# Performance work log

Hardware: AMD Instinct MI355X
Metric: run time of the kernel (lower is better)

The kernel has to match this reference:

```python
import jax, jax.numpy as jnp
import numpy as np

IN_F, OUT_F = 1024, 1024
GRID_SIZE, SPLINE_ORDER = 5, 3
BATCH = 4096
GRID_LO, GRID_HI = -1.0, 1.0


def _make_grid():
    h = (GRID_HI - GRID_LO) / GRID_SIZE
    g = jnp.arange(-SPLINE_ORDER, GRID_SIZE + SPLINE_ORDER + 1, dtype=jnp.float32) * h + GRID_LO  # [12]
    return jnp.broadcast_to(g, (IN_F, g.shape[0]))  # [in, 12]


def setup_inputs() -> dict:
    key = jax.random.key(0)
    k1, k2, k3 = jax.random.split(key, 3)
    x = jax.random.normal(k1, (BATCH, IN_F), dtype=jnp.float32)
    base_weight = jax.random.normal(k2, (OUT_F, IN_F), dtype=jnp.float32) * (1.0 / np.sqrt(IN_F))
    spline_weight = jax.random.normal(k3, (OUT_F, IN_F, GRID_SIZE + SPLINE_ORDER), dtype=jnp.float32) * 0.1
    spline_scaler = jnp.ones((OUT_F, IN_F), dtype=jnp.float32)
    grid = _make_grid()
    return {"x": x, "base_weight": base_weight, "spline_weight": spline_weight,
            "spline_scaler": spline_scaler, "grid": grid}


def b_splines(x, grid):
    # x: [B, in], grid: [in, 12] -> bases: [B, in, grid_size+spline_order]
    xe = x[..., None]  # [B, in, 1]
    bases = ((xe >= grid[:, :-1]) & (xe < grid[:, 1:])).astype(x.dtype)  # [B, in, 11]
    for k in range(1, SPLINE_ORDER + 1):
        t0 = grid[:, :-(k + 1)]
        t1 = grid[:, k:-1]
        t2 = grid[:, k + 1:]
        t3 = grid[:, 1:-k]
        bases = ((xe - t0) / (t1 - t0 + 1e-8) * bases[..., :-1]
                 + (t2 - xe) / (t2 - t3 + 1e-8) * bases[..., 1:])
    return bases


def reference(x, base_weight, spline_weight, spline_scaler, grid):
    base_output = jax.nn.silu(x) @ base_weight.T  # [B, out]
    spline_basis = b_splines(x, grid)             # [B, in, 8]
    spline_output = jnp.einsum('bij,oij,oi->bo', spline_basis, spline_weight, spline_scaler)
    return base_output + spline_output
```

## Files before the change

### kernel.cpp

```cpp
#include <hip/hip_runtime.h>
#include <hip/hip_bf16.h>
#include <stdint.h>
#include <stddef.h>

#define IN_F     1024
#define OUT_F    1024
#define BATCH    4096
#define NSPLINE  8
#define KDIM     (IN_F * 9)
#define GRIDPTS  12

typedef __bf16 bf16;
typedef __bf16 bf16x8 __attribute__((ext_vector_type(8)));
typedef float  f32x4  __attribute__((ext_vector_type(4)));

__global__ __launch_bounds__(256) void build_A(const float* __restrict__ x,
                                               const float* __restrict__ grid,
                                               bf16* __restrict__ A)
{
    __shared__ float g[GRIDPTS];
    __shared__ float rec[33];
    if (threadIdx.x < GRIDPTS) g[threadIdx.x] = grid[threadIdx.x];
    __syncthreads();
    if (threadIdx.x < 33) {
        const int k = threadIdx.x / 11 + 1;
        const int j = threadIdx.x % 11;
        if (j + k <= 11) rec[threadIdx.x] = 1.0f / (g[j + k] - g[j] + 1e-8f);
    }
    __syncthreads();

    const int idx = blockIdx.x * 256 + threadIdx.x;
    const int b = idx >> 10;
    const int i = idx & 1023;
    const float xv = x[idx];

    float bs[11];
#pragma unroll
    for (int j = 0; j < 11; ++j)
        bs[j] = (xv >= g[j] && xv < g[j + 1]) ? 1.0f : 0.0f;

#pragma unroll
    for (int k = 1; k <= 3; ++k) {
        const float* rk = &rec[(k - 1) * 11];
#pragma unroll
        for (int j = 0; j < 10; ++j) {
            if (j <= 10 - k) {
                bs[j] = (xv - g[j]) * rk[j] * bs[j]
                      + (g[j + k + 1] - xv) * rk[j + 1] * bs[j + 1];
            }
        }
    }

    const float si = xv / (1.0f + __expf(-xv));

    bf16* rowp = A + (size_t)b * KDIM;
    rowp[i] = (bf16)si;
#pragma unroll
    for (int j = 0; j < NSPLINE; ++j)
        rowp[(size_t)(j + 1) * IN_F + i] = (bf16)bs[j];
}

__global__ __launch_bounds__(256) void pack_W(const float* __restrict__ bw,
                                              const float* __restrict__ sw,
                                              const float* __restrict__ sc,
                                              bf16* __restrict__ W)
{
    const int idx = blockIdx.x * 256 + threadIdx.x;
    const int i = idx & 1023;
    const float s = sc[idx];

    bf16* rowp = W + (size_t)(idx >> 10) * KDIM;
    rowp[i] = (bf16)bw[idx];

    const float4* swv = (const float4*)(sw + (size_t)idx * NSPLINE);
    const float4 w0 = swv[0];
    const float4 w1 = swv[1];
    rowp[(size_t)1 * IN_F + i] = (bf16)(w0.x * s);
    rowp[(size_t)2 * IN_F + i] = (bf16)(w0.y * s);
    rowp[(size_t)3 * IN_F + i] = (bf16)(w0.z * s);
    rowp[(size_t)4 * IN_F + i] = (bf16)(w0.w * s);
    rowp[(size_t)5 * IN_F + i] = (bf16)(w1.x * s);
    rowp[(size_t)6 * IN_F + i] = (bf16)(w1.y * s);
    rowp[(size_t)7 * IN_F + i] = (bf16)(w1.z * s);
    rowp[(size_t)8 * IN_F + i] = (bf16)(w1.w * s);
}

#define BM8 256
#define BN8 256
#define BK8 64

#define GLOAD_LDS16(gp, lp)                                                          \
    __builtin_amdgcn_global_load_lds((const __attribute__((address_space(1))) void*)(gp), \
                                     (__attribute__((address_space(3))) void*)(lp), 16, 0, 0)

__global__ __launch_bounds__(512, 2) void gemm8(const bf16* __restrict__ A,
                                                const bf16* __restrict__ B,
                                                float* __restrict__ C,
                                                int kLen)
{
    __shared__ bf16 lds[8 * 8192];

    const int tid  = threadIdx.x;
    const int wave = tid >> 6;
    const int lane = tid & 63;

    const int nwg  = gridDim.x;
    const int q    = nwg >> 3;
    const int wgid = (blockIdx.x & 7) * q + (blockIdx.x >> 3);
    const int nxy  = (BATCH / BM8) * (OUT_F / BN8);
    const int z    = wgid / nxy;
    const int rem  = wgid - z * nxy;
    const int by   = rem >> 4;
    const int bx   = rem & 15;

    const int bm = bx * BM8;
    const int bn = by * BN8;
    const int kBase = z * kLen;
    C += (size_t)z * BATCH * OUT_F;

    const int wr = (wave >> 2) * 128;
    const int wc = (wave & 3) * 64;

    f32x4 acc[8][4] = {};

    const int NT   = kLen / BK8;
    const int hmax = 4 * NT;

    const int srow = tid >> 2;
    const int sch  = (((tid & 3) ^ ((tid >> 3) & 3))) * 8;
    const bf16* baseA = A + (size_t)(bm + srow) * KDIM + kBase + sch;
    const bf16* baseB = B + (size_t)(bn + srow) * KDIM + kBase + sch;
    const size_t rstep = (size_t)128 * KDIM;
    bf16* ldsw = &lds[wave * 512];

    auto stage = [&](int h) {
        if (h < hmax) {
            const int t   = h >> 2;
            const int th  = h & 3;
            const int kof = t * BK8 + ((th >> 1) ? 32 : 0);
            const bf16* src = (th & 1) ? baseB : baseA;
            bf16* l0 = ldsw + (h & 7) * 8192;
            GLOAD_LDS16(src + kof, l0);
            GLOAD_LDS16(src + kof + rstep, l0 + 4096);
        }
    };

    for (int h = 0; h < 6; ++h) stage(h);
    asm volatile("s_waitcnt vmcnt(4)" ::: "memory");
    __builtin_amdgcn_s_barrier();

    const int rowk = lane & 15;
    const int kc   = lane >> 4;

#define LDSFRAG(slot, row) (*(const bf16x8*)&lds[(slot) * 8192 + (row) * 32 + \
                               ((kc ^ (((row) >> 1) & 3)) * 8)])

    for (int t = 0; t < NT; ++t) {
        const int h0  = 4 * t;
        const int sA0 = (h0 + 0) & 7, sB0 = (h0 + 1) & 7;
        const int sA1 = (h0 + 2) & 7, sB1 = (h0 + 3) & 7;
        bf16x8 a[4], b[4];

#pragma unroll
        for (int m = 0; m < 4; ++m) a[m] = LDSFRAG(sA0, wr + m * 16 + rowk);
#pragma unroll
        for (int n = 0; n < 4; ++n) b[n] = LDSFRAG(sB0, wc + n * 16 + rowk);
        stage(h0 + 6);
        __builtin_amdgcn_s_barrier();
        asm volatile("s_waitcnt lgkmcnt(0)" ::: "memory");
        __builtin_amdgcn_sched_barrier(0);
        __builtin_amdgcn_s_setprio(1);
#pragma unroll
        for (int m = 0; m < 4; ++m)
#pragma unroll
            for (int n = 0; n < 4; ++n)
                acc[m][n] = __builtin_amdgcn_mfma_f32_16x16x32_bf16(a[m], b[n], acc[m][n], 0, 0, 0);
        __builtin_amdgcn_s_setprio(0);
        __builtin_amdgcn_s_barrier();

#pragma unroll
        for (int m = 0; m < 4; ++m) a[m] = LDSFRAG(sA0, wr + 64 + m * 16 + rowk);
        stage(h0 + 7);
        __builtin_amdgcn_s_barrier();
        asm volatile("s_waitcnt lgkmcnt(0)" ::: "memory");
        __builtin_amdgcn_sched_barrier(0);
        __builtin_amdgcn_s_setprio(1);
#pragma unroll
        for (int m = 0; m < 4; ++m)
#pragma unroll
            for (int n = 0; n < 4; ++n)
                acc[4 + m][n] = __builtin_amdgcn_mfma_f32_16x16x32_bf16(a[m], b[n], acc[4 + m][n], 0, 0, 0);
        __builtin_amdgcn_s_setprio(0);
        __builtin_amdgcn_s_barrier();

#pragma unroll
        for (int m = 0; m < 4; ++m) a[m] = LDSFRAG(sA1, wr + m * 16 + rowk);
#pragma unroll
        for (int n = 0; n < 4; ++n) b[n] = LDSFRAG(sB1, wc + n * 16 + rowk);
        stage(h0 + 8);
        __builtin_amdgcn_s_barrier();
        asm volatile("s_waitcnt lgkmcnt(0)" ::: "memory");
        __builtin_amdgcn_sched_barrier(0);
        __builtin_amdgcn_s_setprio(1);
#pragma unroll
        for (int m = 0; m < 4; ++m)
#pragma unroll
            for (int n = 0; n < 4; ++n)
                acc[m][n] = __builtin_amdgcn_mfma_f32_16x16x32_bf16(a[m], b[n], acc[m][n], 0, 0, 0);
        __builtin_amdgcn_s_setprio(0);
        __builtin_amdgcn_s_barrier();

#pragma unroll
        for (int m = 0; m < 4; ++m) a[m] = LDSFRAG(sA1, wr + 64 + m * 16 + rowk);
        stage(h0 + 9);
        __builtin_amdgcn_s_barrier();
        asm volatile("s_waitcnt lgkmcnt(0)" ::: "memory");
        __builtin_amdgcn_sched_barrier(0);
        __builtin_amdgcn_s_setprio(1);
#pragma unroll
        for (int m = 0; m < 4; ++m)
#pragma unroll
            for (int n = 0; n < 4; ++n)
                acc[4 + m][n] = __builtin_amdgcn_mfma_f32_16x16x32_bf16(a[m], b[n], acc[4 + m][n], 0, 0, 0);
        __builtin_amdgcn_s_setprio(0);
        if (t < NT - 2)       asm volatile("s_waitcnt vmcnt(4)" ::: "memory");
        else if (t == NT - 2) asm volatile("s_waitcnt vmcnt(0)" ::: "memory");
        __builtin_amdgcn_s_barrier();
    }
#undef LDSFRAG

    const int ccol = lane & 15;
    const int crow = (lane >> 4) * 4;
#pragma unroll
    for (int mf = 0; mf < 8; ++mf) {
#pragma unroll
        for (int nf = 0; nf < 4; ++nf) {
            float* cp = C + (size_t)(bm + wr + mf * 16 + crow) * OUT_F + (bn + wc + nf * 16 + ccol);
#pragma unroll
            for (int r = 0; r < 4; ++r)
                cp[(size_t)r * OUT_F] = acc[mf][nf][r];
        }
    }
}

__global__ __launch_bounds__(256) void reduce_partials(const float4* __restrict__ P,
                                                       float4* __restrict__ out,
                                                       int nPart, int n4)
{
    const int stride = gridDim.x * 256;
    for (int i = blockIdx.x * 256 + threadIdx.x; i < n4; i += stride) {
        float4 s = P[i];
        for (int p = 1; p < nPart; ++p) {
            const float4 q = P[(size_t)p * n4 + i];
            s.x += q.x; s.y += q.y; s.z += q.z; s.w += q.w;
        }
        out[i] = s;
    }
}

extern "C" void kernel_launch(void* const* d_in, const int* in_sizes, int n_in,
                              void* d_out, int out_size, void* d_ws, size_t ws_size,
                              hipStream_t stream)
{
    const float* x  = (const float*)d_in[0];
    const float* bw = (const float*)d_in[1];
    const float* sw = (const float*)d_in[2];
    const float* sc = (const float*)d_in[3];
    const float* gr = (const float*)d_in[4];
    float* out = (float*)d_out;

    bf16* A = (bf16*)d_ws;
    bf16* W = A + (size_t)BATCH * KDIM;
    float* parts = (float*)(W + (size_t)OUT_F * KDIM);

    const size_t baseBytes = ((size_t)BATCH + OUT_F) * KDIM * sizeof(bf16);
    const size_t cBytes    = (size_t)BATCH * OUT_F * sizeof(float);

    int split = 1;
    if (ws_size >= baseBytes + 4 * cBytes)      split = 4;
    else if (ws_size >= baseBytes + 2 * cBytes) split = 2;

    build_A<<<(BATCH * IN_F) / 256, 256, 0, stream>>>(x, gr, A);
    pack_W<<<(OUT_F * IN_F) / 256, 256, 0, stream>>>(bw, sw, sc, W);

    const int nblk = (BATCH / BM8) * (OUT_F / BN8) * split;
    float* gemmOut = (split > 1) ? parts : out;
    gemm8<<<nblk, 512, 0, stream>>>(A, W, gemmOut, KDIM / split);

    if (split > 1) {
        const int n4 = BATCH * OUT_F / 4;
        reduce_partials<<<2048, 256, 0, stream>>>((const float4*)parts, (float4*)out,
                                                  split, n4);
    }
}
```

Baseline: 122.9 us.

## Double-buffer LDS fragments in registers to overlap reads with MFMA

Restructures the GEMM main loop so LDS fragment reads for the next MFMA block are issued before the current MFMA block runs. Extra register buffers (a2, b2) and a prologue load make this possible, and the barrier plus lgkmcnt(0) wait before each compute phase is removed. It also hoists the swizzled k-offset into a precomputed value. The aim is to hide LDS latency and cut barrier stalls, at the cost of higher VGPR pressure and reliance on compiler-inserted waits for the LDS reads to complete.

```diff
diff --git a/kernel.cpp b/kernel.cpp
--- a/kernel.cpp
+++ b/kernel.cpp
@@ -114,7 +114,7 @@
     const int bx   = rem & 15;
 
     const int bm = bx * BM8;
-    const int bn = by * BN8;
+    const int bcol = by * BN8;
     const int kBase = z * kLen;
     C += (size_t)z * BATCH * OUT_F;
 
@@ -129,7 +129,7 @@
     const int srow = tid >> 2;
     const int sch  = (((tid & 3) ^ ((tid >> 3) & 3))) * 8;
     const bf16* baseA = A + (size_t)(bm + srow) * KDIM + kBase + sch;
-    const bf16* baseB = B + (size_t)(bn + srow) * KDIM + kBase + sch;
+    const bf16* baseB = B + (size_t)(bcol + srow) * KDIM + kBase + sch;
     const size_t rstep = (size_t)128 * KDIM;
     bf16* ldsw = &lds[wave * 512];
 
@@ -151,23 +151,24 @@
 
     const int rowk = lane & 15;
     const int kc   = lane >> 4;
-
-#define LDSFRAG(slot, row) (*(const bf16x8*)&lds[(slot) * 8192 + (row) * 32 + \
-                               ((kc ^ (((row) >> 1) & 3)) * 8)])
+    const int kxor = (kc ^ ((rowk >> 1) & 3)) * 8;
+
+#define LDSFRAG(slot, row) (*(const bf16x8*)&lds[(slot) * 8192 + (row) * 32 + kxor])
+
+    bf16x8 a[4], b[4], a2[4], b2[4];
+#pragma unroll
+    for (int m = 0; m < 4; ++m) a[m] = LDSFRAG(0, wr + m * 16 + rowk);
+#pragma unroll
+    for (int n = 0; n < 4; ++n) b[n] = LDSFRAG(1, wc + n * 16 + rowk);
 
     for (int t = 0; t < NT; ++t) {
         const int h0  = 4 * t;
-        const int sA0 = (h0 + 0) & 7, sB0 = (h0 + 1) & 7;
+        const int sA0 = (h0 + 0) & 7;
         const int sA1 = (h0 + 2) & 7, sB1 = (h0 + 3) & 7;
-        bf16x8 a[4], b[4];
-
-#pragma unroll
-        for (int m = 0; m < 4; ++m) a[m] = LDSFRAG(sA0, wr + m * 16 + rowk);
-#pragma unroll
-        for (int n = 0; n < 4; ++n) b[n] = LDSFRAG(sB0, wc + n * 16 + rowk);
+
         stage(h0 + 6);
-        __builtin_amdgcn_s_barrier();
-        asm volatile("s_waitcnt lgkmcnt(0)" ::: "memory");
+#pragma unroll
+        for (int m = 0; m < 4; ++m) a2[m] = LDSFRAG(sA0, wr + 64 + m * 16 + rowk);
         __builtin_amdgcn_sched_barrier(0);
         __builtin_amdgcn_s_setprio(1);
 #pragma unroll
@@ -178,53 +179,52 @@
         __builtin_amdgcn_s_setprio(0);
         __builtin_amdgcn_s_barrier();
 
-#pragma unroll
-        for (int m = 0; m < 4; ++m) a[m] = LDSFRAG(sA0, wr + 64 + m * 16 + rowk);
         stage(h0 + 7);
-        __builtin_amdgcn_s_barrier();
-        asm volatile("s_waitcnt lgkmcnt(0)" ::: "memory");
-        __builtin_amdgcn_sched_barrier(0);
-        __builtin_amdgcn_s_setprio(1);
-#pragma unroll
-        for (int m = 0; m < 4; ++m)
-#pragma unroll
-            for (int n = 0; n < 4; ++n)
-                acc[4 + m][n] = __builtin_amdgcn_mfma_f32_16x16x32_bf16(a[m], b[n], acc[4 + m][n], 0, 0, 0);
-        __builtin_amdgcn_s_setprio(0);
-        __builtin_amdgcn_s_barrier();
-
 #pragma unroll
         for (int m = 0; m < 4; ++m) a[m] = LDSFRAG(sA1, wr + m * 16 + rowk);
 #pragma unroll
-        for (int n = 0; n < 4; ++n) b[n] = LDSFRAG(sB1, wc + n * 16 + rowk);
+        for (int n = 0; n < 4; ++n) b2[n] = LDSFRAG(sB1, wc + n * 16 + rowk);
+        __builtin_amdgcn_sched_barrier(0);
+        __builtin_amdgcn_s_setprio(1);
+#pragma unroll
+        for (int m = 0; m < 4; ++m)
+#pragma unroll
+            for (int n = 0; n < 4; ++n)
+                acc[4 + m][n] = __builtin_amdgcn_mfma_f32_16x16x32_bf16(a2[m], b[n], acc[4 + m][n], 0, 0, 0);
+        __builtin_amdgcn_s_setprio(0);
+        __builtin_amdgcn_s_barrier();
+
         stage(h0 + 8);
-        __builtin_amdgcn_s_barrier();
-        asm volatile("s_waitcnt lgkmcnt(0)" ::: "memory");
-        __builtin_amdgcn_sched_barrier(0);
-        __builtin_amdgcn_s_setprio(1);
-#pragma unroll
-        for (int m = 0; m < 4; ++m)
-#pragma unroll
-            for (int n = 0; n < 4; ++n)
-                acc[m][n] = __builtin_amdgcn_mfma_f32_16x16x32_bf16(a[m], b[n], acc[m][n], 0, 0, 0);
-        __builtin_amdgcn_s_setprio(0);
-        __builtin_amdgcn_s_barrier();
-
-#pragma unroll
-        for (int m = 0; m < 4; ++m) a[m] = LDSFRAG(sA1, wr + 64 + m * 16 + rowk);
+#pragma unroll
+        for (int m = 0; m < 4; ++m) a2[m] = LDSFRAG(sA1, wr + 64 + m * 16 + rowk);
+        __builtin_amdgcn_sched_barrier(0);
+        __builtin_amdgcn_s_setprio(1);
+#pragma unroll
+        for (int m = 0; m < 4; ++m)
+#pragma unroll
+            for (int n = 0; n < 4; ++n)
+                acc[m][n] = __builtin_amdgcn_mfma_f32_16x16x32_bf16(a[m], b2[n], acc[m][n], 0, 0, 0);
+        __builtin_amdgcn_s_setprio(0);
+        __builtin_amdgcn_s_barrier();
+
         stage(h0 + 9);
-        __builtin_amdgcn_s_barrier();
-        asm volatile("s_waitcnt lgkmcnt(0)" ::: "memory");
-        __builtin_amdgcn_sched_barrier(0);
-        __builtin_amdgcn_s_setprio(1);
-#pragma unroll
-        for (int m = 0; m < 4; ++m)
-#pragma unroll
-            for (int n = 0; n < 4; ++n)
-                acc[4 + m][n] = __builtin_amdgcn_mfma_f32_16x16x32_bf16(a[m], b[n], acc[4 + m][n], 0, 0, 0);
+        __builtin_amdgcn_sched_barrier(0);
+        __builtin_amdgcn_s_setprio(1);
+#pragma unroll
+        for (int m = 0; m < 4; ++m)
+#pragma unroll
+            for (int n = 0; n < 4; ++n)
+                acc[4 + m][n] = __builtin_amdgcn_mfma_f32_16x16x32_bf16(a2[m], b2[n], acc[4 + m][n], 0, 0, 0);
         __builtin_amdgcn_s_setprio(0);
         if (t < NT - 2)       asm volatile("s_waitcnt vmcnt(4)" ::: "memory");
         else if (t == NT - 2) asm volatile("s_waitcnt vmcnt(0)" ::: "memory");
+        if (t + 1 < NT) {
+            const int nA0 = (h0 + 4) & 7, nB0 = (h0 + 5) & 7;
+#pragma unroll
+            for (int m = 0; m < 4; ++m) a[m] = LDSFRAG(nA0, wr + m * 16 + rowk);
+#pragma unroll
+            for (int n = 0; n < 4; ++n) b[n] = LDSFRAG(nB0, wc + n * 16 + rowk);
+        }
         __builtin_amdgcn_s_barrier();
     }
 #undef LDSFRAG
@@ -235,7 +235,7 @@
     for (int mf = 0; mf < 8; ++mf) {
 #pragma unroll
         for (int nf = 0; nf < 4; ++nf) {
-            float* cp = C + (size_t)(bm + wr + mf * 16 + crow) * OUT_F + (bn + wc + nf * 16 + ccol);
+            float* cp = C + (size_t)(bm + wr + mf * 16 + crow) * OUT_F + (bcol + wc + nf * 16 + ccol);
 #pragma unroll
             for (int r = 0; r < 4; ++r)
                 cp[(size_t)r * OUT_F] = acc[mf][nf][r];
```

New measurement: 122.2 us. About the same (-0.6%).

## Shrink GEMM tile to 128x128 with 4 blocks/CU and split-K of 2

Applied to the files above, without the earlier changes.

Reduces the workgroup tile from 256x256 to 128x128, halving LDS per block and raising the launch-bounds occupancy target to 4 blocks per CU. The main loop is restructured into two stages per K-step with new wait counts, and the split-K factor drops from 4 to 2 so fewer partial outputs must be written and reduced. The smaller tile lowers operand reuse per block and increases global/L2 traffic in exchange for more concurrent blocks and a cheaper reduction.

```diff
diff --git a/kernel.cpp b/kernel.cpp
--- a/kernel.cpp
+++ b/kernel.cpp
@@ -85,20 +85,20 @@
     rowp[(size_t)8 * IN_F + i] = (bf16)(w1.w * s);
 }
 
-#define BM8 256
-#define BN8 256
+#define BM8 128
+#define BN8 128
 #define BK8 64
 
 #define GLOAD_LDS16(gp, lp)                                                          \
     __builtin_amdgcn_global_load_lds((const __attribute__((address_space(1))) void*)(gp), \
                                      (__attribute__((address_space(3))) void*)(lp), 16, 0, 0)
 
-__global__ __launch_bounds__(512, 2) void gemm8(const bf16* __restrict__ A,
+__global__ __launch_bounds__(512, 4) void gemm8(const bf16* __restrict__ A,
                                                 const bf16* __restrict__ B,
                                                 float* __restrict__ C,
                                                 int kLen)
 {
-    __shared__ bf16 lds[8 * 8192];
+    __shared__ bf16 lds[8 * 4096];
 
     const int tid  = threadIdx.x;
     const int wave = tid >> 6;
@@ -110,18 +110,18 @@
     const int nxy  = (BATCH / BM8) * (OUT_F / BN8);
     const int z    = wgid / nxy;
     const int rem  = wgid - z * nxy;
-    const int by   = rem >> 4;
-    const int bx   = rem & 15;
-
-    const int bm = bx * BM8;
-    const int bn = by * BN8;
+    const int by   = rem >> 5;
+    const int bx   = rem & 31;
+
+    const int bm   = bx * BM8;
+    const int bcol = by * BN8;
     const int kBase = z * kLen;
     C += (size_t)z * BATCH * OUT_F;
 
-    const int wr = (wave >> 2) * 128;
-    const int wc = (wave & 3) * 64;
-
-    f32x4 acc[8][4] = {};
+    const int wr = (wave >> 2) * 64;
+    const int wc = (wave & 3) * 32;
+
+    f32x4 acc[4][2] = {};
 
     const int NT   = kLen / BK8;
     const int hmax = 4 * NT;
@@ -129,8 +129,7 @@
     const int srow = tid >> 2;
     const int sch  = (((tid & 3) ^ ((tid >> 3) & 3))) * 8;
     const bf16* baseA = A + (size_t)(bm + srow) * KDIM + kBase + sch;
-    const bf16* baseB = B + (size_t)(bn + srow) * KDIM + kBase + sch;
-    const size_t rstep = (size_t)128 * KDIM;
+    const bf16* baseB = B + (size_t)(bcol + srow) * KDIM + kBase + sch;
     bf16* ldsw = &lds[wave * 512];
 
     auto stage = [&](int h) {
@@ -139,9 +138,7 @@
             const int th  = h & 3;
             const int kof = t * BK8 + ((th >> 1) ? 32 : 0);
             const bf16* src = (th & 1) ? baseB : baseA;
-            bf16* l0 = ldsw + (h & 7) * 8192;
-            GLOAD_LDS16(src + kof, l0);
-            GLOAD_LDS16(src + kof + rstep, l0 + 4096);
+            GLOAD_LDS16(src + kof, ldsw + (h & 7) * 4096);
         }
     };
 
@@ -151,21 +148,23 @@
 
     const int rowk = lane & 15;
     const int kc   = lane >> 4;
-
-#define LDSFRAG(slot, row) (*(const bf16x8*)&lds[(slot) * 8192 + (row) * 32 + \
-                               ((kc ^ (((row) >> 1) & 3)) * 8)])
+    const int kxor = (kc ^ ((rowk >> 1) & 3)) * 8;
+
+#define LDSFRAG(slot, row) (*(const bf16x8*)&lds[(slot) * 4096 + (row) * 32 + kxor])
 
     for (int t = 0; t < NT; ++t) {
         const int h0  = 4 * t;
         const int sA0 = (h0 + 0) & 7, sB0 = (h0 + 1) & 7;
         const int sA1 = (h0 + 2) & 7, sB1 = (h0 + 3) & 7;
-        bf16x8 a[4], b[4];
+        bf16x8 a[4], b[2];
 
 #pragma unroll
         for (int m = 0; m < 4; ++m) a[m] = LDSFRAG(sA0, wr + m * 16 + rowk);
 #pragma unroll
-        for (int n = 0; n < 4; ++n) b[n] = LDSFRAG(sB0, wc + n * 16 + rowk);
+        for (int n = 0; n < 2; ++n) b[n] = LDSFRAG(sB0, wc + n * 16 + rowk);
         stage(h0 + 6);
+        stage(h0 + 7);
+        if (t < NT - 1) asm volatile("s_waitcnt vmcnt(4)" ::: "memory");
         __builtin_amdgcn_s_barrier();
         asm volatile("s_waitcnt lgkmcnt(0)" ::: "memory");
         __builtin_amdgcn_sched_barrier(0);
@@ -173,14 +172,19 @@
 #pragma unroll
         for (int m = 0; m < 4; ++m)
 #pragma unroll
-            for (int n = 0; n < 4; ++n)
+            for (int n = 0; n < 2; ++n)
                 acc[m][n] = __builtin_amdgcn_mfma_f32_16x16x32_bf16(a[m], b[n], acc[m][n], 0, 0, 0);
         __builtin_amdgcn_s_setprio(0);
         __builtin_amdgcn_s_barrier();
 
 #pragma unroll
-        for (int m = 0; m < 4; ++m) a[m] = LDSFRAG(sA0, wr + 64 + m * 16 + rowk);
-        stage(h0 + 7);
+        for (int m = 0; m < 4; ++m) a[m] = LDSFRAG(sA1, wr + m * 16 + rowk);
+#pragma unroll
+        for (int n = 0; n < 2; ++n) b[n] = LDSFRAG(sB1, wc + n * 16 + rowk);
+        stage(h0 + 8);
+        stage(h0 + 9);
+        if (t < NT - 2)       asm volatile("s_waitcnt vmcnt(4)" ::: "memory");
+        else if (t == NT - 2) asm volatile("s_waitcnt vmcnt(0)" ::: "memory");
         __builtin_amdgcn_s_barrier();
         asm volatile("s_waitcnt lgkmcnt(0)" ::: "memory");
         __builtin_amdgcn_sched_barrier(0);
@@ -188,54 +192,20 @@
 #pragma unroll
         for (int m = 0; m < 4; ++m)
 #pragma unroll
-            for (int n = 0; n < 4; ++n)
-                acc[4 + m][n] = __builtin_amdgcn_mfma_f32_16x16x32_bf16(a[m], b[n], acc[4 + m][n], 0, 0, 0);
-        __builtin_amdgcn_s_setprio(0);
-        __builtin_amdgcn_s_barrier();
-
-#pragma unroll
-        for (int m = 0; m < 4; ++m) a[m] = LDSFRAG(sA1, wr + m * 16 + rowk);
-#pragma unroll
-        for (int n = 0; n < 4; ++n) b[n] = LDSFRAG(sB1, wc + n * 16 + rowk);
-        stage(h0 + 8);
-        __builtin_amdgcn_s_barrier();
-        asm volatile("s_waitcnt lgkmcnt(0)" ::: "memory");
-        __builtin_amdgcn_sched_barrier(0);
-        __builtin_amdgcn_s_setprio(1);
-#pragma unroll
-        for (int m = 0; m < 4; ++m)
-#pragma unroll
-            for (int n = 0; n < 4; ++n)
+            for (int n = 0; n < 2; ++n)
                 acc[m][n] = __builtin_amdgcn_mfma_f32_16x16x32_bf16(a[m], b[n], acc[m][n], 0, 0, 0);
         __builtin_amdgcn_s_setprio(0);
         __builtin_amdgcn_s_barrier();
-
-#pragma unroll
-        for (int m = 0; m < 4; ++m) a[m] = LDSFRAG(sA1, wr + 64 + m * 16 + rowk);
-        stage(h0 + 9);
-        __builtin_amdgcn_s_barrier();
-        asm volatile("s_waitcnt lgkmcnt(0)" ::: "memory");
-        __builtin_amdgcn_sched_barrier(0);
-        __builtin_amdgcn_s_setprio(1);
-#pragma unroll
-        for (int m = 0; m < 4; ++m)
-#pragma unroll
-            for (int n = 0; n < 4; ++n)
-                acc[4 + m][n] = __builtin_amdgcn_mfma_f32_16x16x32_bf16(a[m], b[n], acc[4 + m][n], 0, 0, 0);
-        __builtin_amdgcn_s_setprio(0);
-        if (t < NT - 2)       asm volatile("s_waitcnt vmcnt(4)" ::: "memory");
-        else if (t == NT - 2) asm volatile("s_waitcnt vmcnt(0)" ::: "memory");
-        __builtin_amdgcn_s_barrier();
     }
 #undef LDSFRAG
 
     const int ccol = lane & 15;
     const int crow = (lane >> 4) * 4;
 #pragma unroll
-    for (int mf = 0; mf < 8; ++mf) {
-#pragma unroll
-        for (int nf = 0; nf < 4; ++nf) {
-            float* cp = C + (size_t)(bm + wr + mf * 16 + crow) * OUT_F + (bn + wc + nf * 16 + ccol);
+    for (int mf = 0; mf < 4; ++mf) {
+#pragma unroll
+        for (int nf = 0; nf < 2; ++nf) {
+            float* cp = C + (size_t)(bm + wr + mf * 16 + crow) * OUT_F + (bcol + wc + nf * 16 + ccol);
 #pragma unroll
             for (int r = 0; r < 4; ++r)
                 cp[(size_t)r * OUT_F] = acc[mf][nf][r];
@@ -277,8 +247,7 @@
     const size_t cBytes    = (size_t)BATCH * OUT_F * sizeof(float);
 
     int split = 1;
-    if (ws_size >= baseBytes + 4 * cBytes)      split = 4;
-    else if (ws_size >= baseBytes + 2 * cBytes) split = 2;
+    if (ws_size >= baseBytes + 2 * cBytes) split = 2;
 
     build_A<<<(BATCH * IN_F) / 256, 256, 0, stream>>>(x, gr, A);
     pack_W<<<(OUT_F * IN_F) / 256, 256, 0, stream>>>(bw, sw, sc, W);
```

After: 143.4 us. 16.7% more time.
